# Performance work log

Hardware: AMD Instinct MI355X
Metric: run time of the kernel (lower is better)

The kernel has to match this reference:

```python
import jax, jax.numpy as jnp
import numpy as np

N_EMBD = 768
N_HEAD = 12


def setup_inputs() -> dict:
    key = jax.random.key(0)
    ks = jax.random.split(key, 5)
    B, T, C = 8, 1024, N_EMBD
    s_in = 1.0 / np.sqrt(C)
    x = jax.random.normal(ks[0], (B, T, C), dtype=jnp.float32)
    w_attn = jax.random.normal(ks[1], (C, 3 * C), dtype=jnp.float32) * s_in
    b_attn = jnp.zeros((3 * C,), dtype=jnp.float32)
    w_proj = jax.random.normal(ks[2], (C, C), dtype=jnp.float32) * s_in
    b_proj = jnp.zeros((C,), dtype=jnp.float32)
    return {"x": x, "w_attn": w_attn, "b_attn": b_attn,
            "w_proj": w_proj, "b_proj": b_proj}


def reference(x, w_attn, b_attn, w_proj, b_proj):
    B, T, C = x.shape
    H, hs = N_HEAD, C // N_HEAD
    qkv = x @ w_attn + b_attn                      # [B,T,3C]
    q, k, v = jnp.split(qkv, 3, axis=-1)
    # [B,H,T,hs]
    q = q.reshape(B, T, H, hs).transpose(0, 2, 1, 3)
    k = k.reshape(B, T, H, hs).transpose(0, 2, 1, 3)
    v = v.reshape(B, T, H, hs).transpose(0, 2, 1, 3)
    att = jnp.einsum('bhqd,bhkd->bhqk', q, k) * (1.0 / np.sqrt(hs))
    causal = jnp.tril(jnp.ones((T, T), dtype=bool))
    att = jnp.where(causal, att, -jnp.inf)
    att = jax.nn.softmax(att, axis=-1)
    y = jnp.einsum('bhqk,bhkd->bhqd', att, v)      # [B,H,T,hs]
    y = y.transpose(0, 2, 1, 3).reshape(B, T, C)
    return y @ w_proj + b_proj
```

## Files before the change

kernel.cpp:

```cpp
#include <hip/hip_runtime.h>
#include <hip/hip_bf16.h>
#include <stdint.h>

typedef unsigned short u16;
typedef short short8 __attribute__((ext_vector_type(8)));
typedef short short4v __attribute__((ext_vector_type(4)));
typedef float floatx4 __attribute__((ext_vector_type(4)));

__device__ __forceinline__ float b2f(u16 v) {
  union { unsigned int u; float f; } c; c.u = ((unsigned int)v) << 16; return c.f;
}
__device__ __forceinline__ u16 f2b(float f) {
  union { float f; unsigned int u; } c; c.f = f;
  unsigned int u = c.u;
  return (u16)((u + 0x7fffu + ((u >> 16) & 1u)) >> 16);
}

__device__ __forceinline__ void gld_lds16(const u16* g, u16* l) {
  __builtin_amdgcn_global_load_lds(
      (const __attribute__((address_space(1))) unsigned int*)g,
      (__attribute__((address_space(3))) unsigned int*)l,
      16, 0, 0);
}

__device__ __forceinline__ void tile_transpose_f2b(
    const float* __restrict__ in, u16* __restrict__ out,
    int inRS, int outRS, int rb, int cb, int tid)
{
  __shared__ __align__(16) u16 t[64][72];
  const int r = tid >> 2, sg = tid & 3;
  const float* ip = in + (long)(rb + r) * inRS + cb + sg * 16;
#pragma unroll
  for (int i = 0; i < 16; i += 4) {
    float4 f = *(const float4*)(ip + i);
    t[r][sg * 16 + i]     = f2b(f.x);
    t[r][sg * 16 + i + 1] = f2b(f.y);
    t[r][sg * 16 + i + 2] = f2b(f.z);
    t[r][sg * 16 + i + 3] = f2b(f.w);
  }
  __syncthreads();
  short8 v0, v1;
#pragma unroll
  for (int i = 0; i < 8; i++) v0[i] = (short)t[sg * 16 + i][r];
#pragma unroll
  for (int i = 0; i < 8; i++) v1[i] = (short)t[sg * 16 + 8 + i][r];
  *(short8*)(out + (long)(cb + r) * outRS + rb + sg * 16)     = v0;
  *(short8*)(out + (long)(cb + r) * outRS + rb + sg * 16 + 8) = v1;
}

__global__ __launch_bounds__(256) void prep(
    const float* __restrict__ x, u16* __restrict__ xb,
    const float* __restrict__ w_attn, u16* __restrict__ wTa,
    const float* __restrict__ w_proj, u16* __restrict__ wTp)
{
  const int bid = blockIdx.x, tid = threadIdx.x;
  if (bid < 6144) {
    int i = (bid * 256 + tid) * 4;
    float4 f = *(const float4*)(x + i);
    short4v v;
    v[0] = (short)f2b(f.x); v[1] = (short)f2b(f.y);
    v[2] = (short)f2b(f.z); v[3] = (short)f2b(f.w);
    *(short4v*)(xb + i) = v;
  } else if (bid < 6576) {
    int t = bid - 6144;
    tile_transpose_f2b(w_attn, wTa, 2304, 768, (t / 36) * 64, (t % 36) * 64, tid);
  } else {
    int t = bid - 6576;
    tile_transpose_f2b(w_proj, wTp, 768, 768, (t / 12) * 64, (t % 12) * 64, tid);
  }
}

__device__ __forceinline__ void store_out(u16* p, float v)  { *p = f2b(v); }
__device__ __forceinline__ void store_out(float* p, float v) { *p = v; }

template <int BM>
__device__ __forceinline__ void stage(
    const u16* __restrict__ A, const u16* __restrict__ Bt,
    long rowbase, long colbase, int K, int k0,
    u16* dA, u16* dB, int tid)
{
  const int c0 = tid, c1 = tid + 256;
  const int ar0 = c0 >> 2, ak0 = (c0 & 3) * 8;
  const int ar1 = c1 >> 2, ak1 = (c1 & 3) * 8;
  gld_lds16(A + (rowbase + ar0) * K + k0 + ak0, dA + c0 * 8);
  if (BM == 128)
    gld_lds16(A + (rowbase + ar1) * K + k0 + ak1, dA + c1 * 8);
  gld_lds16(Bt + (colbase + ar0) * K + k0 + ak0, dB + c0 * 8);
  gld_lds16(Bt + (colbase + ar1) * K + k0 + ak1, dB + c1 * 8);
}

template <typename OT, int BM, bool SPLIT>
__global__ __launch_bounds__(256) void gemm_bt_bias(
    const u16* __restrict__ A, const u16* __restrict__ Bt,
    const float* __restrict__ bias, OT* __restrict__ C, u16* __restrict__ vT,
    int M, int N, int K, int strideC)
{
  constexpr int WNF = (BM == 128) ? 4 : 2;
  __shared__ __align__(16) u16 sA[2][BM * 32];
  __shared__ __align__(16) u16 sB[2][128 * 32];
  const int tid = threadIdx.x;
  const int lane = tid & 63;
  const int wave = tid >> 6;
  const int wm = (BM == 128) ? (wave >> 1) * 64 : 0;
  const int wn = (BM == 128) ? (wave & 1) * 64 : wave * 32;
  const int l15 = lane & 15;
  const int q = lane >> 4;
  const long rowbase = (long)blockIdx.y * BM;
  const long colbase = (long)blockIdx.x * 128;

  floatx4 acc[4][WNF];
#pragma unroll
  for (int i = 0; i < 4; i++)
#pragma unroll
    for (int j = 0; j < WNF; j++) acc[i][j] = (floatx4){0.f, 0.f, 0.f, 0.f};

  stage<BM>(A, Bt, rowbase, colbase, K, 0, sA[0], sB[0], tid);
  __syncthreads();

  const int NIT = K / 32;
  for (int it = 0; it < NIT; ++it) {
    const int cur = it & 1;
    if (it + 1 < NIT)
      stage<BM>(A, Bt, rowbase, colbase, K, (it + 1) * 32, sA[cur ^ 1], sB[cur ^ 1], tid);
    short8 af[4], bf[WNF];
#pragma unroll
    for (int mt = 0; mt < 4; mt++)
      af[mt] = *(const short8*)(sA[cur] + (wm + mt * 16 + l15) * 32 + q * 8);
#pragma unroll
    for (int nt = 0; nt < WNF; nt++)
      bf[nt] = *(const short8*)(sB[cur] + (wn + nt * 16 + l15) * 32 + q * 8);
#pragma unroll
    for (int mt = 0; mt < 4; mt++)
#pragma unroll
      for (int nt = 0; nt < WNF; nt++)
        acc[mt][nt] = __builtin_amdgcn_mfma_f32_16x16x32_bf16(af[mt], bf[nt], acc[mt][nt], 0, 0, 0);
    if (it + 1 < NIT) __syncthreads();
  }

  if (SPLIT && colbase >= 1536) {
    const long b = rowbase >> 10;
    const int t0b = (int)(rowbase & 1023) + wm;
#pragma unroll
    for (int nt = 0; nt < WNF; nt++) {
      const int col = (int)colbase + wn + nt * 16 + l15;
      const float bv = bias[col];
      const int dloc = col - 1536;
      u16* bp = vT + (b * 12 + (dloc >> 6)) * 65536L + (long)(dloc & 63) * 1024;
#pragma unroll
      for (int mt = 0; mt < 4; mt++) {
        short4v pv;
#pragma unroll
        for (int r = 0; r < 4; r++) pv[r] = (short)f2b(acc[mt][nt][r] + bv);
        *(short4v*)(bp + t0b + mt * 16 + q * 4) = pv;
      }
    }
  } else {
#pragma unroll
    for (int nt = 0; nt < WNF; nt++) {
      const long col = colbase + wn + nt * 16 + l15;
      const float bv = bias[col];
#pragma unroll
      for (int mt = 0; mt < 4; mt++)
#pragma unroll
        for (int r = 0; r < 4; r++) {
          const long row = rowbase + wm + mt * 16 + q * 4 + r;
          store_out(C + row * strideC + col, acc[mt][nt][r] + bv);
        }
    }
  }
}

__global__ __launch_bounds__(256) void attn_fwd(
    const u16* __restrict__ qk, const u16* __restrict__ vT, u16* __restrict__ y)
{
  const int bh = blockIdx.x;
  const int qt = 15 - blockIdx.y;
  const int b = bh / 12, h = bh % 12;
  const long rowOff = (long)b * 1024;
  const int qb = qt * 64;

  __shared__ __align__(16) u16 sK[64 * 72];
  __shared__ __align__(16) u16 sV[2][64 * 72];
  __shared__ __align__(16) u16 sP[64 * 72];

  const int tid = threadIdx.x;
  const int lane = tid & 63, wave = tid >> 6;
  const int l15 = lane & 15, q = lane >> 4;
  const int qrow_g = qb + wave * 16 + l15;

  short8 qf[2];
  {
    const u16* qp = qk + (long)(rowOff + qrow_g) * 1536 + h * 64 + q * 8;
    short8 a0 = *(const short8*)(qp);
    short8 a1 = *(const short8*)(qp + 32);
#pragma unroll
    for (int i = 0; i < 8; i++) {
      a0[i] = (short)f2b(b2f((u16)a0[i]) * 0.125f);
      a1[i] = (short)f2b(b2f((u16)a1[i]) * 0.125f);
    }
    qf[0] = a0; qf[1] = a1;
  }

  float m_i = -1e30f, l_i = 0.f;
  floatx4 o[4];
#pragma unroll
  for (int nt = 0; nt < 4; nt++) o[nt] = (floatx4){0.f, 0.f, 0.f, 0.f};

  for (int j = 0; j <= qt; j++) {
    const int jb = j * 64;
    u16* sVc = sV[j & 1];
#pragma unroll
    for (int rep = 0; rep < 2; rep++) {
      int idx = tid + rep * 256;
      int r = idx >> 3, ch = (idx & 7) * 8;
      *(short8*)(sK + r * 72 + ch) =
          *(const short8*)(qk + (long)(rowOff + jb + r) * 1536 + 768 + h * 64 + ch);
      *(short8*)(sVc + r * 72 + ch) =
          *(const short8*)(vT + (long)bh * 65536 + (long)r * 1024 + jb + ch);
    }
    __syncthreads();

    floatx4 sf[4];
#pragma unroll
    for (int mt = 0; mt < 4; mt++) sf[mt] = (floatx4){0.f, 0.f, 0.f, 0.f};
#pragma unroll
    for (int kk = 0; kk < 2; kk++) {
#pragma unroll
      for (int mt = 0; mt < 4; mt++) {
        short8 kf = *(const short8*)(sK + (mt * 16 + l15) * 72 + kk * 32 + q * 8);
        sf[mt] = __builtin_amdgcn_mfma_f32_16x16x32_bf16(kf, qf[kk], sf[mt], 0, 0, 0);
      }
    }

    float mx = m_i;
#pragma unroll
    for (int mt = 0; mt < 4; mt++)
#pragma unroll
      for (int r = 0; r < 4; r++) {
        int key_g = jb + mt * 16 + q * 4 + r;
        float v = sf[mt][r];
        if (key_g > qrow_g) v = -1e30f;
        sf[mt][r] = v;
        mx = fmaxf(mx, v);
      }
    mx = fmaxf(mx, __shfl_xor(mx, 16));
    mx = fmaxf(mx, __shfl_xor(mx, 32));
    float al = __expf(m_i - mx);
    m_i = mx;
    float rsum = 0.f;
#pragma unroll
    for (int mt = 0; mt < 4; mt++) {
      short4v pv;
#pragma unroll
      for (int r = 0; r < 4; r++) {
        float p = __expf(sf[mt][r] - mx);
        rsum += p;
        pv[r] = (short)f2b(p);
      }
      *(short4v*)(sP + (wave * 16 + l15) * 72 + mt * 16 + q * 4) = pv;
    }
    rsum += __shfl_xor(rsum, 16);
    rsum += __shfl_xor(rsum, 32);
    l_i = l_i * al + rsum;
    __syncthreads();

    float al_r[4];
#pragma unroll
    for (int r = 0; r < 4; r++) al_r[r] = __shfl(al, q * 4 + r);
#pragma unroll
    for (int nt = 0; nt < 4; nt++)
#pragma unroll
      for (int r = 0; r < 4; r++) o[nt][r] *= al_r[r];
#pragma unroll
    for (int kk = 0; kk < 2; kk++) {
      short8 pf = *(const short8*)(sP + (wave * 16 + l15) * 72 + kk * 32 + q * 8);
#pragma unroll
      for (int nt = 0; nt < 4; nt++) {
        short8 vf = *(const short8*)(sVc + (nt * 16 + l15) * 72 + kk * 32 + q * 8);
        o[nt] = __builtin_amdgcn_mfma_f32_16x16x32_bf16(pf, vf, o[nt], 0, 0, 0);
      }
    }
  }

  float linv = 1.f / l_i;
  float li_r[4];
#pragma unroll
  for (int r = 0; r < 4; r++) li_r[r] = __shfl(linv, q * 4 + r);
#pragma unroll
  for (int nt = 0; nt < 4; nt++)
#pragma unroll
    for (int r = 0; r < 4; r++) {
      int row = qb + wave * 16 + q * 4 + r;
      int col = h * 64 + nt * 16 + l15;
      y[(rowOff + row) * 768 + col] = f2b(o[nt][r] * li_r[r]);
    }
}

extern "C" void kernel_launch(void* const* d_in, const int* in_sizes, int n_in,
                              void* d_out, int out_size, void* d_ws, size_t ws_size,
                              hipStream_t stream) {
  const float* x      = (const float*)d_in[0];
  const float* w_attn = (const float*)d_in[1];
  const float* b_attn = (const float*)d_in[2];
  const float* w_proj = (const float*)d_in[3];
  const float* b_proj = (const float*)d_in[4];
  float* out = (float*)d_out;

  char* ws = (char*)d_ws;
  u16* xb   = (u16*)ws; ws += (size_t)8192 * 768 * 2;
  u16* wTa  = (u16*)ws; ws += (size_t)2304 * 768 * 2;
  u16* wTp  = (u16*)ws; ws += (size_t)768 * 768 * 2;
  u16* qk   = (u16*)ws; ws += (size_t)8192 * 1536 * 2;
  u16* vT   = (u16*)ws; ws += (size_t)96 * 64 * 1024 * 2;
  u16* yatt = (u16*)ws; ws += (size_t)8192 * 768 * 2;

  prep<<<dim3(6720), 256, 0, stream>>>(x, xb, w_attn, wTa, w_proj, wTp);

  gemm_bt_bias<u16, 128, true><<<dim3(18, 64), 256, 0, stream>>>(
      xb, wTa, b_attn, qk, vT, 8192, 2304, 768, 1536);

  attn_fwd<<<dim3(96, 16), 256, 0, stream>>>(qk, vT, yatt);

  gemm_bt_bias<float, 64, false><<<dim3(6, 128), 256, 0, stream>>>(
      yatt, wTp, b_proj, out, (u16*)nullptr, 8192, 768, 768, 768);
}
```

Before: 211.6 us.

## Split-K output projection with atomics and skip causal masking off-diagonal

The output projection GEMM now splits K into three chunks across grid z and accumulates into the float output with atomicAdd. The output is pre-filled with the bias in the prep kernel, which gains 6144 extra blocks. Separately, the attention kernel applies the causal mask only on the diagonal tile and uses a plain max elsewhere. The split-K path raises block count for the small projection GEMM, at the cost of scalar atomic traffic and an extra bias write pass.

```diff
diff --git a/kernel.cpp b/kernel.cpp
--- a/kernel.cpp
+++ b/kernel.cpp
@@ -51,7 +51,8 @@
 __global__ __launch_bounds__(256) void prep(
     const float* __restrict__ x, u16* __restrict__ xb,
     const float* __restrict__ w_attn, u16* __restrict__ wTa,
-    const float* __restrict__ w_proj, u16* __restrict__ wTp)
+    const float* __restrict__ w_proj, u16* __restrict__ wTp,
+    const float* __restrict__ b_proj, float* __restrict__ out)
 {
   const int bid = blockIdx.x, tid = threadIdx.x;
   if (bid < 6144) {
@@ -64,9 +65,12 @@
   } else if (bid < 6576) {
     int t = bid - 6144;
     tile_transpose_f2b(w_attn, wTa, 2304, 768, (t / 36) * 64, (t % 36) * 64, tid);
-  } else {
+  } else if (bid < 6720) {
     int t = bid - 6576;
     tile_transpose_f2b(w_proj, wTp, 768, 768, (t / 12) * 64, (t % 12) * 64, tid);
+  } else {
+    int i = ((bid - 6720) * 256 + tid) * 4;
+    *(float4*)(out + i) = *(const float4*)(b_proj + (i % 768));
   }
 }
 
@@ -89,7 +93,7 @@
   gld_lds16(Bt + (colbase + ar1) * K + k0 + ak1, dB + c1 * 8);
 }
 
-template <typename OT, int BM, bool SPLIT>
+template <typename OT, int BM, int MODE>
 __global__ __launch_bounds__(256) void gemm_bt_bias(
     const u16* __restrict__ A, const u16* __restrict__ Bt,
     const float* __restrict__ bias, OT* __restrict__ C, u16* __restrict__ vT,
@@ -107,6 +111,8 @@
   const int q = lane >> 4;
   const long rowbase = (long)blockIdx.y * BM;
   const long colbase = (long)blockIdx.x * 128;
+  const int kchunk = (MODE == 2) ? K / gridDim.z : K;
+  const int kbase  = (MODE == 2) ? blockIdx.z * kchunk : 0;
 
   floatx4 acc[4][WNF];
 #pragma unroll
@@ -114,14 +120,14 @@
 #pragma unroll
     for (int j = 0; j < WNF; j++) acc[i][j] = (floatx4){0.f, 0.f, 0.f, 0.f};
 
-  stage<BM>(A, Bt, rowbase, colbase, K, 0, sA[0], sB[0], tid);
+  stage<BM>(A, Bt, rowbase, colbase, K, kbase, sA[0], sB[0], tid);
   __syncthreads();
 
-  const int NIT = K / 32;
+  const int NIT = kchunk / 32;
   for (int it = 0; it < NIT; ++it) {
     const int cur = it & 1;
     if (it + 1 < NIT)
-      stage<BM>(A, Bt, rowbase, colbase, K, (it + 1) * 32, sA[cur ^ 1], sB[cur ^ 1], tid);
+      stage<BM>(A, Bt, rowbase, colbase, K, kbase + (it + 1) * 32, sA[cur ^ 1], sB[cur ^ 1], tid);
     short8 af[4], bf[WNF];
 #pragma unroll
     for (int mt = 0; mt < 4; mt++)
@@ -137,7 +143,7 @@
     if (it + 1 < NIT) __syncthreads();
   }
 
-  if (SPLIT && colbase >= 1536) {
+  if (MODE == 1 && colbase >= 1536) {
     const long b = rowbase >> 10;
     const int t0b = (int)(rowbase & 1023) + wm;
 #pragma unroll
@@ -153,6 +159,18 @@
         for (int r = 0; r < 4; r++) pv[r] = (short)f2b(acc[mt][nt][r] + bv);
         *(short4v*)(bp + t0b + mt * 16 + q * 4) = pv;
       }
+    }
+  } else if (MODE == 2) {
+#pragma unroll
+    for (int nt = 0; nt < WNF; nt++) {
+      const long col = colbase + wn + nt * 16 + l15;
+#pragma unroll
+      for (int mt = 0; mt < 4; mt++)
+#pragma unroll
+        for (int r = 0; r < 4; r++) {
+          const long row = rowbase + wm + mt * 16 + q * 4 + r;
+          atomicAdd((float*)C + row * strideC + col, acc[mt][nt][r]);
+        }
     }
   } else {
 #pragma unroll
@@ -233,16 +251,23 @@
     }
 
     float mx = m_i;
-#pragma unroll
-    for (int mt = 0; mt < 4; mt++)
-#pragma unroll
-      for (int r = 0; r < 4; r++) {
-        int key_g = jb + mt * 16 + q * 4 + r;
-        float v = sf[mt][r];
-        if (key_g > qrow_g) v = -1e30f;
-        sf[mt][r] = v;
-        mx = fmaxf(mx, v);
-      }
+    if (j == qt) {
+#pragma unroll
+      for (int mt = 0; mt < 4; mt++)
+#pragma unroll
+        for (int r = 0; r < 4; r++) {
+          int key_g = jb + mt * 16 + q * 4 + r;
+          float v = sf[mt][r];
+          if (key_g > qrow_g) v = -1e30f;
+          sf[mt][r] = v;
+          mx = fmaxf(mx, v);
+        }
+    } else {
+#pragma unroll
+      for (int mt = 0; mt < 4; mt++)
+#pragma unroll
+        for (int r = 0; r < 4; r++) mx = fmaxf(mx, sf[mt][r]);
+    }
     mx = fmaxf(mx, __shfl_xor(mx, 16));
     mx = fmaxf(mx, __shfl_xor(mx, 32));
     float al = __expf(m_i - mx);
@@ -314,13 +339,13 @@
   u16* vT   = (u16*)ws; ws += (size_t)96 * 64 * 1024 * 2;
   u16* yatt = (u16*)ws; ws += (size_t)8192 * 768 * 2;
 
-  prep<<<dim3(6720), 256, 0, stream>>>(x, xb, w_attn, wTa, w_proj, wTp);
-
-  gemm_bt_bias<u16, 128, true><<<dim3(18, 64), 256, 0, stream>>>(
+  prep<<<dim3(12864), 256, 0, stream>>>(x, xb, w_attn, wTa, w_proj, wTp, b_proj, out);
+
+  gemm_bt_bias<u16, 128, 1><<<dim3(18, 64), 256, 0, stream>>>(
       xb, wTa, b_attn, qk, vT, 8192, 2304, 768, 1536);
 
   attn_fwd<<<dim3(96, 16), 256, 0, stream>>>(qk, vT, yatt);
 
-  gemm_bt_bias<float, 64, false><<<dim3(6, 128), 256, 0, stream>>>(
+  gemm_bt_bias<float, 64, 2><<<dim3(6, 128, 3), 256, 0, stream>>>(
       yatt, wTp, b_proj, out, (u16*)nullptr, 8192, 768, 768, 768);
 }
```

New measurement: 256.6 us. 21.3% more time.
